# Optimization experiments

Hardware: AMD Instinct MI355X
Metric: run time of the kernel (lower is better)

The kernel has to match this reference:

```python
import jax, jax.numpy as jnp
import numpy as np

WINDOW = 7
SHIFT = 3
NUM_HEADS = 12
DIM = 384
FFN = 4 * DIM
EPS = 1e-5


def _rel_pos_index(w):
    coords = np.stack(np.meshgrid(np.arange(w), np.arange(w), indexing='ij'))  # [2,w,w]
    flat = coords.reshape(2, -1)
    rel = (flat[:, :, None] - flat[:, None, :]).transpose(1, 2, 0)  # [w*w, w*w, 2]
    rel[..., 0] += w - 1
    rel[..., 1] += w - 1
    rel[..., 0] *= 2 * w - 1
    return rel.sum(-1).astype(np.int32)  # [w*w, w*w]


def _attn_mask(hp, wp, w, s):
    # replicate get_attn_mask: region labeling, window partition, pairwise diff
    img = np.zeros((hp, wp), dtype=np.float32)
    cnt = 0
    for hs in (slice(0, -w), slice(-w, -s), slice(-s, None)):
        for ws in (slice(0, -w), slice(-w, -s), slice(-s, None)):
            img[hs, ws] = cnt
            cnt += 1
    mw = img.reshape(hp // w, w, wp // w, w).transpose(0, 2, 1, 3).reshape(-1, w * w)
    diff = mw[:, None, :] - mw[:, :, None]  # unsqueeze(1) - unsqueeze(2)
    return jnp.asarray(np.where(diff != 0, -100.0, 0.0).astype(np.float32))


def _ln(x, g, b):
    mu = jnp.mean(x, -1, keepdims=True)
    var = jnp.mean(jnp.square(x - mu), -1, keepdims=True)
    return (x - mu) * jax.lax.rsqrt(var + EPS) * g + b


def setup_inputs() -> dict:
    key = jax.random.key(0)
    ks = jax.random.split(key, 12)
    B, H, W, C = 8, 56, 56, DIM
    sd = 0.02
    inp = {
        'hidden_states': jax.random.normal(ks[0], (B, H * W, C), jnp.float32),
        'ln1_g': jnp.ones((C,), jnp.float32), 'ln1_b': jnp.zeros((C,), jnp.float32),
        'q_w': jax.random.normal(ks[1], (C, C), jnp.float32) * sd, 'q_b': jnp.zeros((C,), jnp.float32),
        'k_w': jax.random.normal(ks[2], (C, C), jnp.float32) * sd, 'k_b': jnp.zeros((C,), jnp.float32),
        'v_w': jax.random.normal(ks[3], (C, C), jnp.float32) * sd, 'v_b': jnp.zeros((C,), jnp.float32),
        'rpb_table': jax.random.normal(ks[4], ((2 * WINDOW - 1) ** 2, NUM_HEADS), jnp.float32) * sd,
        'rp_index': jnp.asarray(_rel_pos_index(WINDOW)),
        'proj_w': jax.random.normal(ks[5], (C, C), jnp.float32) * sd, 'proj_b': jnp.zeros((C,), jnp.float32),
        'ln2_g': jnp.ones((C,), jnp.float32), 'ln2_b': jnp.zeros((C,), jnp.float32),
        'fc1_w': jax.random.normal(ks[6], (C, FFN), jnp.float32) * sd, 'fc1_b': jnp.zeros((FFN,), jnp.float32),
        'fc2_w': jax.random.normal(ks[7], (FFN, C), jnp.float32) * sd, 'fc2_b': jnp.zeros((C,), jnp.float32),
        'height': H, 'width': W,
    }
    return inp


def reference(hidden_states, ln1_g, ln1_b, q_w, q_b, k_w, k_b, v_w, v_b,
              rpb_table, rp_index, proj_w, proj_b, ln2_g, ln2_b,
              fc1_w, fc1_b, fc2_w, fc2_b, height, width):
    w, s, nh = WINDOW, SHIFT, NUM_HEADS
    B, L, C = hidden_states.shape
    hd = C // nh
    shortcut = hidden_states

    x = _ln(hidden_states, ln1_g, ln1_b).reshape(B, height, width, C)
    pad_b = (w - height % w) % w
    pad_r = (w - width % w) % w
    if pad_b or pad_r:
        x = jnp.pad(x, ((0, 0), (0, pad_b), (0, pad_r), (0, 0)))
    Hp, Wp = height + pad_b, width + pad_r

    if s > 0:
        x = jnp.roll(x, shift=(-s, -s), axis=(1, 2))

    # window partition -> [B*nW, w*w, C]
    N = w * w
    xw = x.reshape(B, Hp // w, w, Wp // w, w, C).transpose(0, 1, 3, 2, 4, 5).reshape(-1, N, C)

    q = (xw @ q_w + q_b).reshape(-1, N, nh, hd).transpose(0, 2, 1, 3)
    k = (xw @ k_w + k_b).reshape(-1, N, nh, hd).transpose(0, 2, 1, 3)
    v = (xw @ v_w + v_b).reshape(-1, N, nh, hd).transpose(0, 2, 1, 3)

    scores = jnp.einsum('whnd,whmd->whnm', q, k) / jnp.sqrt(jnp.float32(hd))
    bias = rpb_table[rp_index.reshape(-1)].reshape(N, N, nh).transpose(2, 0, 1)
    scores = scores + bias[None]

    if s > 0:
        mask = _attn_mask(Hp, Wp, w, s)  # [nW, N, N]
        nW = mask.shape[0]
        scores = scores.reshape(B, nW, nh, N, N) + mask[None, :, None]
        scores = scores.reshape(-1, nh, N, N)

    probs = jax.nn.softmax(scores, axis=-1)
    ctx = jnp.einsum('whnm,whmd->whnd', probs, v).transpose(0, 2, 1, 3).reshape(-1, N, C)
    attn_out = ctx @ proj_w + proj_b

    # window reverse
    xr = attn_out.reshape(B, Hp // w, Wp // w, w, w, C).transpose(0, 1, 3, 2, 4, 5).reshape(B, Hp, Wp, C)
    if s > 0:
        xr = jnp.roll(xr, shift=(s, s), axis=(1, 2))
    if pad_b or pad_r:
        xr = xr[:, :height, :width, :]
    xr = xr.reshape(B, height * width, C)

    h = shortcut + xr
    y = _ln(h, ln2_g, ln2_b)
    y = jax.nn.gelu(y @ fc1_w + fc1_b, approximate=False)
    return h + (y @ fc2_w + fc2_b)
```

## Files before the change

### kernel.cpp

```cpp
#include <hip/hip_runtime.h>
#include <hip/hip_bf16.h>

typedef unsigned short u16;
typedef short bf16x8 __attribute__((ext_vector_type(8)));
typedef float f32x4 __attribute__((ext_vector_type(4)));

__device__ __forceinline__ u16 f2bf(float x) {
  __hip_bfloat16 h = __float2bfloat16(x);
  return *reinterpret_cast<u16*>(&h);
}
__device__ __forceinline__ float bf2f(u16 x) {
  __hip_bfloat16 h = *reinterpret_cast<__hip_bfloat16*>(&x);
  return __bfloat162float(h);
}
__device__ __forceinline__ float rdany(const void* p, size_t i, int f) {
  return f ? ((const float*)p)[i] : bf2f(((const u16*)p)[i]);
}

__device__ __forceinline__ void gld_lds16(const u16* g, u16* l) {
  __builtin_amdgcn_global_load_lds(
      (const __attribute__((address_space(1))) void*)g,
      (__attribute__((address_space(3))) void*)l, 16, 0, 0);
}

__device__ __forceinline__ float gelu_fast(float x) {
  float z = fabsf(x) * 0.70710678118654752f;
  float t = 1.f / (1.f + 0.3275911f * z);
  float p = t * (0.254829592f +
            t * (-0.284496736f +
            t * (1.421413741f +
            t * (-1.453152027f + t * 1.061405429f))));
  float er = 1.f - p * __expf(-z * z);
  er = (x < 0.f) ? -er : er;
  return 0.5f * x * (1.f + er);
}

__global__ void detect_k(const u16* __restrict__ ln1g_raw, int* __restrict__ flag) {
  if (threadIdx.x == 0 && blockIdx.x == 0)
    *flag = (ln1g_raw[0] == 0 && ln1g_raw[2] == 0) ? 1 : 0;
}

__global__ __launch_bounds__(256) void prep_k(
    const void* qw, const void* kw, const void* vw, const void* pw,
    const void* f1w, const void* f2w,
    u16* __restrict__ qwT, u16* __restrict__ kwT, u16* __restrict__ vwT,
    u16* __restrict__ pwT, u16* __restrict__ f1T, u16* __restrict__ f2T,
    const void* s0, const void* s1, const void* s2, const void* s3,
    const void* s4, const void* s5, const void* s6, const void* s7,
    const void* s8, const void* s9, const void* s10,
    u16* __restrict__ vecdst, const int* __restrict__ rpi,
    u16* __restrict__ biasT, const int* __restrict__ flag) {
  int f = *flag;
  int b = blockIdx.x;
  if (b >= 1728) {
    int tid = threadIdx.y * 32 + threadIdx.x;
    if (b == 1729) {
      for (int i = tid; i < 28812; i += 256) {
        int hh = i / 2401, r = i - hh * 2401;
        biasT[i] = f2bf(rdany(s10, (size_t)rpi[r] * 12 + hh, f));
      }
      return;
    }
    const void* srcs[11] = {s0, s1, s2, s3, s4, s5, s6, s7, s8, s9, s10};
    const int offs[12] = {0, 384, 768, 1152, 1536, 1920, 2304, 2688, 3072, 3456, 4992, 7020};
    for (int i = tid; i < 7020; i += 256) {
      int seg = 0;
#pragma unroll
      for (int t = 1; t < 11; t++) seg += (i >= offs[t]) ? 1 : 0;
      vecdst[i] = f2bf(rdany(srcs[seg], i - offs[seg], f));
    }
    return;
  }
  const void* src; u16* dst; int R, C, bx, by;
  if (b < 576) {
    int m = b / 144, t = b - m * 144;
    src = (m == 0) ? qw : (m == 1) ? kw : (m == 2) ? vw : pw;
    dst = (m == 0) ? qwT : (m == 1) ? kwT : (m == 2) ? vwT : pwT;
    R = 384; C = 384; bx = t % 12; by = t / 12;
  } else if (b < 1152) {
    int t = b - 576; src = f1w; dst = f1T; R = 384; C = 1536;
    bx = t % 48; by = t / 48;
  } else {
    int t = b - 1152; src = f2w; dst = f2T; R = 1536; C = 384;
    bx = t % 12; by = t / 12;
  }
  __shared__ u16 tbuf[32][33];
  int x = threadIdx.x, y = threadIdx.y;
  int gx = bx * 32, gy = by * 32;
#pragma unroll
  for (int j = 0; j < 32; j += 8)
    tbuf[y + j][x] = f2bf(rdany(src, (size_t)(gy + y + j) * C + gx + x, f));
  __syncthreads();
#pragma unroll
  for (int j = 0; j < 32; j += 8) dst[(size_t)(gx + y + j) * R + gy + x] = tbuf[x][y + j];
}

__global__ __launch_bounds__(256) void ln1_window_k(
    const void* __restrict__ hid, const u16* __restrict__ g,
    const u16* __restrict__ b, u16* __restrict__ xw, int rowoff,
    const int* __restrict__ flag) {
  int f = *flag;
  int wv = threadIdx.x >> 6, lane = threadIdx.x & 63;
  int lrow = blockIdx.x * 4 + wv;
  int row = rowoff + lrow;
  int wid = row / 49, n = row - wid * 49;
  int bimg = wid >> 6, w8 = wid & 63;
  int wi = w8 >> 3, wj = w8 & 7;
  int p = n / 7, q = n - p * 7;
  int si = wi * 7 + p + 3; if (si >= 56) si -= 56;
  int sj = wj * 7 + q + 3; if (sj >= 56) sj -= 56;
  size_t src = ((size_t)bimg * 3136 + si * 56 + sj) * 384;
  float x[6]; float s = 0.f, s2 = 0.f;
#pragma unroll
  for (int e = 0; e < 6; e++) {
    x[e] = rdany(hid, src + e * 64 + lane, f);
    s += x[e]; s2 += x[e] * x[e];
  }
#pragma unroll
  for (int off = 32; off; off >>= 1) { s += __shfl_xor(s, off); s2 += __shfl_xor(s2, off); }
  float mu = s * (1.f / 384.f);
  float var = s2 * (1.f / 384.f) - mu * mu;
  float rs = 1.f / sqrtf(var + 1e-5f);
  size_t dst = (size_t)lrow * 384;
#pragma unroll
  for (int e = 0; e < 6; e++) {
    int c = e * 64 + lane;
    float yv = (x[e] - mu) * rs * bf2f(g[c]) + bf2f(b[c]);
    xw[dst + c] = f2bf(yv);
  }
}

__global__ __launch_bounds__(256) void ln2_k(
    const float* hsrc, const u16* __restrict__ g,
    const u16* __restrict__ b, u16* __restrict__ out) {
  int wv = threadIdx.x >> 6, lane = threadIdx.x & 63;
  int row = blockIdx.x * 4 + wv;
  size_t src = (size_t)row * 384;
  float x[6]; float s = 0.f, s2 = 0.f;
#pragma unroll
  for (int e = 0; e < 6; e++) {
    x[e] = hsrc[src + e * 64 + lane];
    s += x[e]; s2 += x[e] * x[e];
  }
#pragma unroll
  for (int off = 32; off; off >>= 1) { s += __shfl_xor(s, off); s2 += __shfl_xor(s2, off); }
  float mu = s * (1.f / 384.f);
  float var = s2 * (1.f / 384.f) - mu * mu;
  float rs = 1.f / sqrtf(var + 1e-5f);
#pragma unroll
  for (int e = 0; e < 6; e++) {
    int c = e * 64 + lane;
    float yv = (x[e] - mu) * rs * bf2f(g[c]) + bf2f(b[c]);
    out[src + c] = f2bf(yv);
  }
}

template <int EPI>
__global__ __launch_bounds__(256, 4) void gemm_bt(
    const u16* __restrict__ A, const u16* __restrict__ Bt,
    const u16* __restrict__ bias, void* outB,
    const void* __restrict__ shortcut, const float* hres,
    int M, int N, int K, int gmoff, int gx, const int* __restrict__ flag) {
  __shared__ __align__(16) u16 As[2][128 * 32];
  __shared__ __align__(16) u16 Bs[2][128 * 32];
  int bx = blockIdx.x;
  if (bx >= gx) return;
  int tid = threadIdx.x;
  int m0 = bx * 128, n0 = blockIdx.y * 128;
  int lane = tid & 63, wv = tid >> 6;
  int wm = (wv >> 1) * 64, wn = (wv & 1) * 64;
  int l15 = lane & 15, quad = lane >> 4;
  f32x4 acc[4][4];
#pragma unroll
  for (int a = 0; a < 4; a++)
#pragma unroll
    for (int c = 0; c < 4; c++) acc[a][c] = (f32x4){0.f, 0.f, 0.f, 0.f};

  int rowS[2], cS[2], wbS[2];
#pragma unroll
  for (int i = 0; i < 2; i++) {
    int id = i * 256 + tid;
    rowS[i] = id >> 2;
    cS[i] = id & 3;
    wbS[i] = (id & ~63) * 8;
  }

#define STAGE(buf, kb_)                                                       \
  {                                                                           \
    _Pragma("unroll") for (int i = 0; i < 2; i++) {                           \
      gld_lds16(A + (size_t)(m0 + rowS[i]) * K + (kb_) + cS[i] * 8,           \
                &As[buf][wbS[i]]);                                            \
      gld_lds16(Bt + (size_t)(n0 + rowS[i]) * K + (kb_) + cS[i] * 8,          \
                &Bs[buf][wbS[i]]);                                            \
    }                                                                         \
  }

  STAGE(0, 0);
  int cur = 0;
  for (int kb = 0; kb < K; kb += 32) {
    if (kb + 32 < K) {
      STAGE(cur ^ 1, kb + 32);
      asm volatile("s_waitcnt vmcnt(4)" ::: "memory");
    } else {
      asm volatile("s_waitcnt vmcnt(0)" ::: "memory");
    }
    __builtin_amdgcn_s_barrier();
    __builtin_amdgcn_sched_barrier(0);
    __builtin_amdgcn_s_setprio(1);
    {
      bf16x8 af[4], bfv[4];
#pragma unroll
      for (int mi = 0; mi < 4; mi++)
        af[mi] = *(const bf16x8*)&As[cur][(wm + mi * 16 + l15) * 32 + quad * 8];
#pragma unroll
      for (int ni = 0; ni < 4; ni++)
        bfv[ni] = *(const bf16x8*)&Bs[cur][(wn + ni * 16 + l15) * 32 + quad * 8];
#pragma unroll
      for (int mi = 0; mi < 4; mi++)
#pragma unroll
        for (int ni = 0; ni < 4; ni++)
          acc[mi][ni] = __builtin_amdgcn_mfma_f32_16x16x32_bf16(af[mi], bfv[ni], acc[mi][ni], 0, 0, 0);
    }
    __builtin_amdgcn_s_setprio(0);
    __builtin_amdgcn_sched_barrier(0);
    __builtin_amdgcn_s_barrier();
    cur ^= 1;
  }
#undef STAGE

  int f = (EPI == 2) ? *flag : 0;
  float biasv[4];
#pragma unroll
  for (int ni = 0; ni < 4; ni++) biasv[ni] = bf2f(bias[n0 + wn + ni * 16 + l15]);
  int seg = n0 / 384;
#pragma unroll
  for (int mi = 0; mi < 4; mi++) {
#pragma unroll
    for (int r = 0; r < 4; r++) {
      int gm = m0 + wm + mi * 16 + quad * 4 + r;
      size_t orow = 0;
      if (EPI == 2) {
        int grow = gmoff + gm;
        int wid = grow / 49, nIn = grow - wid * 49;
        int bimg = wid >> 6, w8 = wid & 63;
        int wi = w8 >> 3, wj = w8 & 7;
        int p = nIn / 7, q = nIn - p * 7;
        int oi = wi * 7 + p + 3; if (oi >= 56) oi -= 56;
        int oj = wj * 7 + q + 3; if (oj >= 56) oj -= 56;
        orow = ((size_t)bimg * 3136 + oi * 56 + oj) * 384;
      }
#pragma unroll
      for (int ni = 0; ni < 4; ni++) {
        int gn = n0 + wn + ni * 16 + l15;
        float v = acc[mi][ni][r] + biasv[ni];
        if (EPI == 1) {
          v = gelu_fast(v);
          ((u16*)outB)[(size_t)gm * N + gn] = f2bf(v);
        } else if (EPI == 2) {
          float hv = rdany(shortcut, orow + gn, f) + v;
          hv = fminf(fmaxf(hv, -1000.f), 1000.f);
          ((float*)outB)[orow + gn] = hv;
        } else if (EPI == 3) {
          float t = v + hres[(size_t)gm * N + gn];
          t = fminf(fmaxf(t, -1000.f), 1000.f);
          ((float*)outB)[(size_t)gm * N + gn] = t;
        } else {
          u16* dst = (u16*)outB + (size_t)seg * M * 384;
          dst[(size_t)gm * 384 + (gn - seg * 384)] = f2bf(v);
        }
      }
    }
  }
}

__global__ __launch_bounds__(256, 5) void attn_k(
    const u16* __restrict__ Q, const u16* __restrict__ Kb, const u16* __restrict__ V,
    const u16* __restrict__ biasT, u16* __restrict__ ctx, int wdoff) {
  __shared__ __align__(16) u16 qs[64 * 56];
  __shared__ __align__(16) u16 ks_[64 * 56];
  __shared__ __align__(16) u16 vt[32 * 72];
  __shared__ __align__(16) u16 P[64 * 72];
  __shared__ int regid[49];
  int lwd = blockIdx.x, hh = blockIdx.y;
  int wd = wdoff + lwd;
  int tid = threadIdx.x;
  int w8 = wd & 63, wi = w8 >> 3, wj = w8 & 7;

  for (int idx = tid; idx < 840; idx += 256) {
    int rr = idx / 56, cc = idx - rr * 56;
    qs[(49 + rr) * 56 + cc] = 0;
    ks_[(49 + rr) * 56 + cc] = 0;
  }
  for (int idx = tid; idx < 480; idx += 256) {
    int d = idx / 15, m = 49 + (idx - d * 15);
    vt[d * 72 + m] = 0;
  }
  if (tid < 49) {
    int p = tid / 7, q = tid - p * 7;
    int rr = (wi == 7) ? (p < 4 ? 1 : 2) : 0;
    int cc = (wj == 7) ? (q < 4 ? 1 : 2) : 0;
    regid[tid] = rr * 3 + cc;
  }
  size_t base = ((size_t)lwd * 49) * 384 + hh * 32;
  for (int idx = tid; idx < 392; idx += 256) {
    int mat = idx >= 196;
    int rid = idx - mat * 196;
    int n = rid >> 2, c = rid & 3;
    uint4 val = *(const uint4*)((mat ? Kb : Q) + base + (size_t)n * 384 + c * 8);
    *(uint4*)&((mat ? ks_ : qs)[n * 56 + c * 8]) = val;
  }
  for (int idx = tid; idx < 196; idx += 256) {
    int n = idx >> 2, c = idx & 3;
    uint4 val = *(const uint4*)(V + base + (size_t)n * 384 + c * 8);
    u16 tmp[8];
    *(uint4*)tmp = val;
#pragma unroll
    for (int t = 0; t < 8; t++) vt[(c * 8 + t) * 72 + n] = tmp[t];
  }
  __syncthreads();

  int lane = tid & 63, wv = tid >> 6, l15 = lane & 15, quad = lane >> 4;
  f32x4 zero = (f32x4){0.f, 0.f, 0.f, 0.f};
  bf16x8 aq = *(const bf16x8*)&qs[(wv * 16 + l15) * 56 + quad * 8];
  f32x4 sc[4];
#pragma unroll
  for (int mi = 0; mi < 4; mi++) {
    bf16x8 bk = *(const bf16x8*)&ks_[(mi * 16 + l15) * 56 + quad * 8];
    sc[mi] = __builtin_amdgcn_mfma_f32_16x16x32_bf16(aq, bk, zero, 0, 0, 0);
  }
  const float scale = 0.17677669529663687f;

  int rm[4];
#pragma unroll
  for (int mi = 0; mi < 4; mi++) {
    int m = mi * 16 + l15;
    rm[mi] = (m < 49) ? regid[m] : -2;
  }
  float pv[4][4];
#pragma unroll
  for (int r = 0; r < 4; r++) {
    int n = wv * 16 + quad * 4 + r;
    int rn = (n < 49) ? regid[n] : -1;
    const u16* brow = biasT + hh * 2401 + n * 49;
#pragma unroll
    for (int mi = 0; mi < 4; mi++) {
      int m = mi * 16 + l15;
      float v = sc[mi][r] * scale;
      if (n < 49 && m < 49) {
        v += bf2f(brow[m]);
        if (rn != rm[mi]) v -= 100.f;
      }
      if (m >= 49) v = -1e4f;
      pv[r][mi] = v;
    }
    float mx = fmaxf(fmaxf(pv[r][0], pv[r][1]), fmaxf(pv[r][2], pv[r][3]));
#pragma unroll
    for (int off = 1; off < 16; off <<= 1) mx = fmaxf(mx, __shfl_xor(mx, off));
    float sum = 0.f;
#pragma unroll
    for (int mi = 0; mi < 4; mi++) {
      pv[r][mi] = __expf(pv[r][mi] - mx);
      sum += pv[r][mi];
    }
#pragma unroll
    for (int off = 1; off < 16; off <<= 1) sum += __shfl_xor(sum, off);
    float inv = 1.f / sum;
#pragma unroll
    for (int mi = 0; mi < 4; mi++)
      P[n * 72 + mi * 16 + l15] = f2bf(pv[r][mi] * inv);
  }

  f32x4 oacc[2]; oacc[0] = zero; oacc[1] = zero;
#pragma unroll
  for (int ks = 0; ks < 2; ks++) {
    bf16x8 ap = *(const bf16x8*)&P[(wv * 16 + l15) * 72 + ks * 32 + quad * 8];
#pragma unroll
    for (int ni = 0; ni < 2; ni++) {
      bf16x8 bv = *(const bf16x8*)&vt[(ni * 16 + l15) * 72 + ks * 32 + quad * 8];
      oacc[ni] = __builtin_amdgcn_mfma_f32_16x16x32_bf16(ap, bv, oacc[ni], 0, 0, 0);
    }
  }
#pragma unroll
  for (int ni = 0; ni < 2; ni++) {
#pragma unroll
    for (int r = 0; r < 4; r++) {
      int n = wv * 16 + quad * 4 + r;
      if (n < 49) {
        int d = ni * 16 + l15;
        ctx[base + (size_t)n * 384 + d] = f2bf(oacc[ni][r]);
      }
    }
  }
}

static inline int pad8(int gx) { return (gx + 7) & ~7; }

extern "C" void kernel_launch(void* const* d_in, const int* in_sizes, int n_in,
                              void* d_out, int out_size, void* d_ws, size_t ws_size,
                              hipStream_t stream) {
  const void* hid = d_in[0];
  const void* ln1g = d_in[1];
  const void* ln1b = d_in[2];
  const void* qw = d_in[3];
  const void* qb = d_in[4];
  const void* kw = d_in[5];
  const void* kbias = d_in[6];
  const void* vw = d_in[7];
  const void* vb = d_in[8];
  const void* rpb = d_in[9];
  const int* rpi = (const int*)d_in[10];
  const void* pw = d_in[11];
  const void* pb = d_in[12];
  const void* ln2g = d_in[13];
  const void* ln2b = d_in[14];
  const void* f1w = d_in[15];
  const void* f1b = d_in[16];
  const void* f2w = d_in[17];
  const void* f2b = d_in[18];

  char* ws = (char*)d_ws;
  u16* wT = (u16*)ws;
  u16* qwT = wT;
  u16* kwT = qwT + 147456;
  u16* vwT = kwT + 147456;
  u16* pwT = vwT + 147456;
  u16* f1T = pwT + 147456;
  u16* f2T = f1T + 589824;
  u16* VEC = (u16*)(ws + 3538944);
  u16* s_ln1g = VEC + 0;
  u16* s_ln1b = VEC + 384;
  u16* s_qkvb = VEC + 768;
  u16* s_pb = VEC + 1920;
  u16* s_ln2g = VEC + 2304;
  u16* s_ln2b = VEC + 2688;
  u16* s_f2b = VEC + 3072;
  u16* s_f1b = VEC + 3456;
  u16* s_rpb = VEC + 4992;
  int* flag = (int*)(ws + 3552984);
  u16* biasT = (u16*)(ws + 3552992);
  const size_t head = 3610624;

  size_t avail = (ws_size > head) ? ws_size - head : 0;
  int rows1 = (avail >= (size_t)25088 * 3072) ? 25088
            : (avail >= (size_t)12544 * 3072) ? 12544 : 6272;
  int rows2 = (avail >= (size_t)25088 * 3840) ? 25088
            : (avail >= (size_t)12544 * 3840) ? 12544 : 3584;

  u16* P1 = (u16*)(ws + head);
  u16* xw = P1;
  u16* Qb = P1 + (size_t)rows1 * 384;
  u16* Kb = Qb + (size_t)rows1 * 384;
  u16* Vb = Kb + (size_t)rows1 * 384;
  u16* y2 = P1;
  u16* f1o = P1 + (size_t)rows2 * 384;
  float* hbuf = (float*)d_out;

  detect_k<<<1, 64, 0, stream>>>((const u16*)ln1g, flag);
  dim3 tb(32, 8);
  prep_k<<<1730, tb, 0, stream>>>(qw, kw, vw, pw, f1w, f2w,
                                  qwT, kwT, vwT, pwT, f1T, f2T,
                                  ln1g, ln1b, qb, kbias, vb, pb, ln2g, ln2b,
                                  f2b, f1b, rpb, VEC, rpi, biasT, flag);

  for (int off = 0; off < 25088; off += rows1) {
    int gx = rows1 / 128;
    ln1_window_k<<<rows1 / 4, 256, 0, stream>>>(hid, s_ln1g, s_ln1b, xw, off, flag);
    gemm_bt<4><<<dim3(pad8(gx), 9), 256, 0, stream>>>(
        xw, qwT, s_qkvb, Qb, nullptr, nullptr, rows1, 1152, 384, 0, gx, flag);
    attn_k<<<dim3(rows1 / 49, 12), 256, 0, stream>>>(Qb, Kb, Vb, biasT, xw, off / 49);
    gemm_bt<2><<<dim3(pad8(gx), 3), 256, 0, stream>>>(
        xw, pwT, s_pb, hbuf, hid, nullptr, rows1, 384, 384, off, gx, flag);
  }

  for (int off = 0; off < 25088; off += rows2) {
    int gx = rows2 / 128;
    ln2_k<<<rows2 / 4, 256, 0, stream>>>(hbuf + (size_t)off * 384, s_ln2g, s_ln2b, y2);
    gemm_bt<1><<<dim3(pad8(gx), 12), 256, 0, stream>>>(
        y2, f1T, s_f1b, f1o, nullptr, nullptr, rows2, 1536, 384, 0, gx, flag);
    gemm_bt<3><<<dim3(pad8(gx), 3), 256, 0, stream>>>(
        f1o, f2T, s_f2b, hbuf + (size_t)off * 384, nullptr,
        hbuf + (size_t)off * 384, rows2, 384, 1536, 0, gx, flag);
  }
}
```

Measured before the change: 401.5 us.

## Use tanh-form GELU and precompute incremented GEMM load pointers

Replaces the erf-polynomial GELU with the tanh approximation, written as a sigmoid identity using one exp and one reciprocal. Separately, the GEMM main loop now keeps running A/B global pointers that advance by 32 each step instead of recomputing full row-times-K address products on every stage. The GELU swap cuts per-element epilogue math but changes numerics from exact erf GELU to the tanh approximation, which adds error. The pointer change trims integer address arithmetic in the hot loop.

```diff
diff --git a/kernel.cpp b/kernel.cpp
--- a/kernel.cpp
+++ b/kernel.cpp
@@ -24,15 +24,11 @@
 }
 
 __device__ __forceinline__ float gelu_fast(float x) {
-  float z = fabsf(x) * 0.70710678118654752f;
-  float t = 1.f / (1.f + 0.3275911f * z);
-  float p = t * (0.254829592f +
-            t * (-0.284496736f +
-            t * (1.421413741f +
-            t * (-1.453152027f + t * 1.061405429f))));
-  float er = 1.f - p * __expf(-z * z);
-  er = (x < 0.f) ? -er : er;
-  return 0.5f * x * (1.f + er);
+  float x2 = x * x;
+  float u2 = 1.5957691216057308f * x * __builtin_fmaf(0.044715f, x2, 1.f);
+  float e = __expf(u2);
+  float r = 1.f / (e + 1.f);
+  return x - x * r;
 }
 
 __global__ void detect_k(const u16* __restrict__ ln1g_raw, int* __restrict__ flag) {
@@ -184,22 +180,31 @@
     cS[i] = id & 3;
     wbS[i] = (id & ~63) * 8;
   }
-
-#define STAGE(buf, kb_)                                                       \
-  {                                                                           \
-    _Pragma("unroll") for (int i = 0; i < 2; i++) {                           \
-      gld_lds16(A + (size_t)(m0 + rowS[i]) * K + (kb_) + cS[i] * 8,           \
-                &As[buf][wbS[i]]);                                            \
-      gld_lds16(Bt + (size_t)(n0 + rowS[i]) * K + (kb_) + cS[i] * 8,          \
-                &Bs[buf][wbS[i]]);                                            \
-    }                                                                         \
-  }
-
-  STAGE(0, 0);
+  const u16* pA[2]; const u16* pB[2];
+#pragma unroll
+  for (int i = 0; i < 2; i++) {
+    pA[i] = A + (size_t)(m0 + rowS[i]) * K + cS[i] * 8;
+    pB[i] = Bt + (size_t)(n0 + rowS[i]) * K + cS[i] * 8;
+  }
+
+#pragma unroll
+  for (int i = 0; i < 2; i++) {
+    gld_lds16(pA[i], &As[0][wbS[i]]);
+    gld_lds16(pB[i], &Bs[0][wbS[i]]);
+  }
+#pragma unroll
+  for (int i = 0; i < 2; i++) { pA[i] += 32; pB[i] += 32; }
+
   int cur = 0;
   for (int kb = 0; kb < K; kb += 32) {
     if (kb + 32 < K) {
-      STAGE(cur ^ 1, kb + 32);
+#pragma unroll
+      for (int i = 0; i < 2; i++) {
+        gld_lds16(pA[i], &As[cur ^ 1][wbS[i]]);
+        gld_lds16(pB[i], &Bs[cur ^ 1][wbS[i]]);
+      }
+#pragma unroll
+      for (int i = 0; i < 2; i++) { pA[i] += 32; pB[i] += 32; }
       asm volatile("s_waitcnt vmcnt(4)" ::: "memory");
     } else {
       asm volatile("s_waitcnt vmcnt(0)" ::: "memory");
@@ -226,7 +231,6 @@
     __builtin_amdgcn_s_barrier();
     cur ^= 1;
   }
-#undef STAGE
 
   int f = (EPI == 2) ? *flag : 0;
   float biasv[4];
```

New measurement: 397.1 us. Within noise of the previous version (-1.1%).
